# Kernel tuning notes

Measured on AMD Instinct MI355X. Metric: run time of the kernel, lower is better.

## Reference

```python
import jax, jax.numpy as jnp
import numpy as np

N = 65536          # n_pts
K = 16             # n_neighbours
IN_DIM, HID, OUT_DIM = 128, 1024, 32


def setup_inputs() -> dict:
    key = jax.random.key(0)
    ks = jax.random.split(key, 16)

    def lin(k, i, o):
        kw, kb = jax.random.split(k)
        s = 1.0 / np.sqrt(i)
        return (jax.random.uniform(kw, (i, o), jnp.float32, -s, s),
                jax.random.uniform(kb, (o,), jnp.float32, -s, s))

    W1, b1 = lin(ks[0], IN_DIM, HID)
    W2, b2 = lin(ks[1], HID, HID)
    W3, b3 = lin(ks[2], HID, HID // 2)
    W4, b4 = lin(ks[3], HID // 2, OUT_DIM)

    x1 = jax.random.normal(ks[4], (N, IN_DIM), jnp.float32)
    x2 = jax.random.normal(ks[5], (N, IN_DIM), jnp.float32)
    # faiss.knn_gpu outputs (distances, neighbor indices) -- modeled as inputs
    dists1 = jax.random.uniform(ks[6], (N, K), jnp.float32)
    dists2 = jax.random.uniform(ks[7], (N, K), jnp.float32)
    nn_idx1 = jax.random.randint(ks[8], (N, K), 0, N)
    nn_idx2 = jax.random.randint(ks[9], (N, K), 0, N)

    return {"x1": x1, "x2": x2, "dists1": dists1, "nn_idx1": nn_idx1,
            "dists2": dists2, "nn_idx2": nn_idx2,
            "W1": W1, "b1": b1, "W2": W2, "b2": b2,
            "W3": W3, "b3": b3, "W4": W4, "b4": b4}


def _mapper(x, W1, b1, W2, b2, W3, b3, W4, b4):
    h = jax.nn.relu(x @ W1 + b1)
    h = jax.nn.relu(h @ W2 + b2)
    h = jax.nn.relu(h @ W3 + b3)
    return h @ W4 + b4


def _degree(dists, nn_flat, rows_flat):
    # Gaussian edge weights w = exp(-d^2 / (2 sigma^2)), sigma = row mean of d.
    # Symmetrized COO affinity A has entries (nn, row) and (row, nn) each w/2.
    # Row-sum of A (= torch.sparse.sum(A, dim=1)); by symmetry also the col-sum.
    sigma = dists.mean(axis=1, keepdims=True)
    w = jnp.exp(-dists ** 2 / (2.0 * sigma ** 2)).reshape(-1)
    wh = 0.5 * w
    d = (jax.ops.segment_sum(wh, rows_flat, num_segments=N)
         + jax.ops.segment_sum(wh, nn_flat, num_segments=N))
    return d


def reference(x1, x2, dists1, nn_idx1, dists2, nn_idx2,
              W1, b1, W2, b2, W3, b3, W4, b4):
    rows_flat = jnp.repeat(jnp.arange(N, dtype=nn_idx1.dtype), K)
    nn1_flat = nn_idx1.reshape(-1)
    nn2_flat = nn_idx2.reshape(-1)

    # --- ort step on x1 (eval pass) ---
    y1 = _mapper(x1, W1, b1, W2, b2, W3, b3, W4, b4)
    d1 = _degree(dists1, nn1_flat, rows_flat)
    y1 = y1 / d1[:, None]
    gram = y1.T @ y1 + 1e-7 * jnp.eye(OUT_DIM, dtype=y1.dtype)
    L = jnp.linalg.cholesky(gram)
    operator = jnp.linalg.inv(L).T * jnp.asarray(np.sqrt(N), y1.dtype)

    # --- loss pass on x2 ---
    d2 = _degree(dists2, nn2_flat, rows_flat)  # col-sum of affinity A2
    y = _mapper(x2, W1, b1, W2, b2, W3, b3, W4, b4) @ operator
    y = y / d2[:, None]

    # per-edge squared embedding distances ||y_i - y_{nn(i,k)}||^2  [N,K]
    diff = y[:, None, :] - y[nn_idx2]          # [N, K, OUT_DIM]
    de = jnp.sum(diff * diff, axis=-1).reshape(-1)
    # sparse D has entries (nn,row) and (row,nn) each with value de.
    # total sum of A @ D == colsum(A) . rowsum(D)  (duplicates sum in COO).
    rowsum_D = (jax.ops.segment_sum(de, nn2_flat, num_segments=N)
                + jax.ops.segment_sum(de, rows_flat, num_segments=N))
    loss = jnp.dot(d2, rowsum_D) / N
    return loss
```

## Files before the change

kernel.cpp:

```cpp
#include <hip/hip_runtime.h>


#define NPTS  65536
#define KNN   16
#define INDIM 128
#define HID   1024
#define HID2  512
#define ODIM  32
#define ESL   32

typedef unsigned short u16;
typedef unsigned int   u32;
typedef __attribute__((ext_vector_type(8))) short bf16x8;
typedef __attribute__((ext_vector_type(4))) float f32x4;

__device__ __forceinline__ u16 f2bf(float v) {
    union { float f; unsigned u; } x; x.f = v;
    unsigned r = x.u + 0x7fffu + ((x.u >> 16) & 1u);
    return (u16)(r >> 16);
}

__device__ __forceinline__ void gload_lds16(const u16* g, u16* l) {
    __builtin_amdgcn_global_load_lds(
        (const __attribute__((address_space(1))) u32*)g,
        (__attribute__((address_space(3))) u32*)l, 16, 0, 0);
}

template <int N> __device__ __forceinline__ void vmwait() {
    asm volatile("s_waitcnt vmcnt(%0)" :: "n"(N) : "memory");
}
__device__ __forceinline__ void wg_barrier() {
    asm volatile("s_barrier" ::: "memory");
}

__global__ void cvt_bf16_k(const float* __restrict__ in, u16* __restrict__ out, int n4) {
    int i = blockIdx.x * blockDim.x + threadIdx.x;
    if (i >= n4) return;
    float4 v = reinterpret_cast<const float4*>(in)[i];
    unsigned lo = (unsigned)f2bf(v.x) | ((unsigned)f2bf(v.y) << 16);
    unsigned hi = (unsigned)f2bf(v.z) | ((unsigned)f2bf(v.w) << 16);
    reinterpret_cast<uint2*>(out)[i] = make_uint2(lo, hi);
}

__global__ void trans_bf16_k(const float* __restrict__ W, u16* __restrict__ Wt,
                             int rows, int cols) {
    int idx = blockIdx.x * blockDim.x + threadIdx.x;
    if (idx >= rows * cols) return;
    int o = idx / rows, i = idx - o * rows;
    Wt[idx] = f2bf(W[(size_t)i * cols + o]);
}

__global__ void edgew_k(const float* __restrict__ dists1, float* __restrict__ w1,
                        float* __restrict__ dr1,
                        const float* __restrict__ dists2, float* __restrict__ w2,
                        float* __restrict__ dr2) {
    const float* dists = blockIdx.y ? dists2 : dists1;
    float*       wbuf  = blockIdx.y ? w2     : w1;
    float*       drow  = blockIdx.y ? dr2    : dr1;
    int i = blockIdx.x * blockDim.x + threadIdx.x;
    if (i >= NPTS) return;
    const float4* dr = reinterpret_cast<const float4*>(dists + (size_t)i * KNN);
    float4 a = dr[0], b = dr[1], c = dr[2], e = dr[3];
    float buf[KNN] = {a.x,a.y,a.z,a.w,b.x,b.y,b.z,b.w,c.x,c.y,c.z,c.w,e.x,e.y,e.z,e.w};
    float s = 0.f;
    #pragma unroll
    for (int k = 0; k < KNN; ++k) s += buf[k];
    float sigma = s * (1.f / KNN);
    float inv2s2 = 1.f / (2.f * sigma * sigma);
    float w[KNN];
    float rs = 0.f;
    #pragma unroll
    for (int k = 0; k < KNN; ++k) { w[k] = __expf(-buf[k] * buf[k] * inv2s2); rs += w[k]; }
    drow[i] = 0.5f * rs;
    float4* wo = reinterpret_cast<float4*>(wbuf + (size_t)i * KNN);
    wo[0] = make_float4(w[0], w[1], w[2], w[3]);
    wo[1] = make_float4(w[4], w[5], w[6], w[7]);
    wo[2] = make_float4(w[8], w[9], w[10], w[11]);
    wo[3] = make_float4(w[12], w[13], w[14], w[15]);
}

__global__ __launch_bounds__(512) void scatter_k(
    const int* __restrict__ nn1, const float* __restrict__ w1,
    const int* __restrict__ nn2, const float* __restrict__ w2,
    float* __restrict__ partial) {
    __shared__ float bins[16384];
    const int slice = blockIdx.x, range = blockIdx.y, g = blockIdx.z;
    const int* nn   = g ? nn2 : nn1;
    const float* wb = g ? w2  : w1;
    for (int b = threadIdx.x; b < 16384; b += 512) bins[b] = 0.f;
    __syncthreads();
    const int per4  = (NPTS * KNN / ESL) >> 2;
    const int base4 = slice * per4;
    const int4*   nn4 = reinterpret_cast<const int4*>(nn);
    const float4* w4  = reinterpret_cast<const float4*>(wb);
    #pragma unroll 2
    for (int k = 0; k < per4 / 512; ++k) {
        int e4 = base4 + k * 512 + threadIdx.x;
        int4   idx = nn4[e4];
        float4 wv  = w4[e4];
        if ((idx.x >> 14) == range) atomicAdd(&bins[idx.x & 16383], wv.x);
        if ((idx.y >> 14) == range) atomicAdd(&bins[idx.y & 16383], wv.y);
        if ((idx.z >> 14) == range) atomicAdd(&bins[idx.z & 16383], wv.z);
        if ((idx.w >> 14) == range) atomicAdd(&bins[idx.w & 16383], wv.w);
    }
    __syncthreads();
    float* dst = partial + ((size_t)(g * ESL + slice) << 16) + (range << 14);
    for (int b = threadIdx.x; b < 16384; b += 512) dst[b] = bins[b];
}

__global__ __launch_bounds__(256) void dreduce_k(
    const float* __restrict__ partial, float* __restrict__ d1, float* __restrict__ d2) {
    int i = blockIdx.x * 256 + threadIdx.x;
    int g = blockIdx.y;
    const float* p = partial + ((size_t)(g * ESL) << 16) + i;
    float s = 0.f;
    #pragma unroll 8
    for (int sl = 0; sl < ESL; ++sl) s += p[(size_t)sl << 16];
    float* d = g ? d2 : d1;
    d[i] += 0.5f * s;
}

template <int BN, bool RELU>
__global__ __launch_bounds__(512) void gemm256_k(
    const u16* __restrict__ A, const u16* __restrict__ Bt,
    const float* __restrict__ bias, u16* __restrict__ C,
    int M, int Ncols, int Kd)
{
    constexpr int WN   = BN / 4;
    constexpr int NREP = WN / 16;
    constexpr int AL   = 4;
    constexpr int BL   = BN / 64;
    constexpr int LQ   = AL + BL;

    constexpr int A_U16  = 2 * 256 * 64;
    constexpr int B_U16  = 2 * BN * 64;
    constexpr int LDSC   = BN + 16;
    constexpr int EP_U16 = 256 * LDSC;
    constexpr int SM_U16 = (A_U16 + B_U16 > EP_U16) ? (A_U16 + B_U16) : EP_U16;

    __shared__ __attribute__((aligned(16))) u16 smem[SM_U16];
    u16* Asm = smem;
    u16* Bsm = smem + A_U16;

    const int tid  = threadIdx.x;
    const int lane = tid & 63;
    const int wave = tid >> 6;
    const int wr   = wave >> 2;
    const int wc   = wave & 3;
    const int l15  = lane & 15;
    const int kq   = lane >> 4;

    const int nwg = gridDim.x * gridDim.y;
    int sid = blockIdx.y * gridDim.x + blockIdx.x;
    int q = nwg >> 3, r = nwg & 7;
    int xcd = sid & 7, ix = sid >> 3;
    int logical = (xcd < r) ? xcd * (q + 1) + ix
                            : r * (q + 1) + (xcd - r) * q + ix;
    const int m0 = (logical / gridDim.x) * 256;
    const int n0 = (logical % gridDim.x) * BN;

    const int lrow = lane >> 3;
    const int lcol = ((lane & 7) ^ lrow) * 8;

    auto stage = [&](int slot, int kt) {
        #pragma unroll
        for (int j = 0; j < AL; ++j) {
            int seg = wave * AL + j;
            gload_lds16(A + (size_t)(m0 + seg * 8 + lrow) * Kd + kt + lcol,
                        &Asm[slot * 256 * 64 + seg * 512]);
        }
        #pragma unroll
        for (int j = 0; j < BL; ++j) {
            int seg = wave * BL + j;
            gload_lds16(Bt + (size_t)(n0 + seg * 8 + lrow) * Kd + kt + lcol,
                        &Bsm[slot * BN * 64 + seg * 512]);
        }
    };
    auto rdA = [&](int slot, int mi, int ks) -> bf16x8 {
        int row = wr * 128 + mi * 16 + l15;
        int ch  = (ks * 4 + kq) ^ (row & 7);
        return *reinterpret_cast<const bf16x8*>(&Asm[slot * 256 * 64 + row * 64 + ch * 8]);
    };
    auto rdB = [&](int slot, int ni, int ks) -> bf16x8 {
        int row = wc * WN + ni * 16 + l15;
        int ch  = (ks * 4 + kq) ^ (row & 7);
        return *reinterpret_cast<const bf16x8*>(&Bsm[slot * BN * 64 + row * 64 + ch * 8]);
    };

    const int NT = Kd >> 6;
    f32x4 acc[8][NREP] = {};

    stage(0, 0);
    for (int t = 0; t < NT; ++t) {
        const int cur = t & 1;
        if (t + 1 < NT) { stage(cur ^ 1, (t + 1) << 6); vmwait<LQ>(); }
        else            { vmwait<0>(); }
        wg_barrier();

        bf16x8 a[8][2], b[NREP][2];
        #pragma unroll
        for (int mi = 0; mi < 8; ++mi) { a[mi][0] = rdA(cur, mi, 0); a[mi][1] = rdA(cur, mi, 1); }
        #pragma unroll
        for (int ni = 0; ni < NREP; ++ni) { b[ni][0] = rdB(cur, ni, 0); b[ni][1] = rdB(cur, ni, 1); }
        __builtin_amdgcn_s_setprio(1);
        #pragma unroll
        for (int mi = 0; mi < 8; ++mi)
            #pragma unroll
            for (int ni = 0; ni < NREP; ++ni) {
                acc[mi][ni] = __builtin_amdgcn_mfma_f32_16x16x32_bf16(a[mi][0], b[ni][0], acc[mi][ni], 0, 0, 0);
                acc[mi][ni] = __builtin_amdgcn_mfma_f32_16x16x32_bf16(a[mi][1], b[ni][1], acc[mi][ni], 0, 0, 0);
            }
        __builtin_amdgcn_s_setprio(0);
        wg_barrier();
    }

    #pragma unroll
    for (int ni = 0; ni < NREP; ++ni) {
        int col = wc * WN + ni * 16 + l15;
        float bv = bias[n0 + col];
        #pragma unroll
        for (int mi = 0; mi < 8; ++mi)
            #pragma unroll
            for (int r2 = 0; r2 < 4; ++r2) {
                int row = wr * 128 + mi * 16 + kq * 4 + r2;
                float v = acc[mi][ni][r2] + bv;
                if (RELU) v = v > 0.f ? v : 0.f;
                smem[row * LDSC + col] = f2bf(v);
            }
    }
    __syncthreads();
    constexpr int CHUNKS = BN / 8;
    constexpr int ITERS  = 256 * CHUNKS / 512;
    #pragma unroll
    for (int it = 0; it < ITERS; ++it) {
        int task = it * 512 + tid;
        int row  = task / CHUNKS;
        int ch   = task % CHUNKS;
        uint4 v = *reinterpret_cast<const uint4*>(&smem[row * LDSC + ch * 8]);
        *reinterpret_cast<uint4*>(&C[(size_t)(m0 + row) * Ncols + n0 + ch * 8]) = v;
    }
}

__global__ __launch_bounds__(256) void layer4_k(
    const u16* __restrict__ A, const u16* __restrict__ Bt,
    const float* __restrict__ bias, const float* __restrict__ dscale,
    float* __restrict__ Y, int M)
{
    __shared__ __attribute__((aligned(16))) u16 Bs[32 * 520];
    int tid = threadIdx.x;
    #pragma unroll
    for (int j = 0; j < 8; ++j) {
        int cch = tid + j * 256;
        int row = cch >> 6;
        int ko  = (cch & 63) * 8;
        *reinterpret_cast<uint4*>(&Bs[row * 520 + ko]) =
            *reinterpret_cast<const uint4*>(Bt + (size_t)row * 512 + ko);
    }
    __syncthreads();
    int lane = tid & 63, wave = tid >> 6;
    int l15 = lane & 15, kq = lane >> 4;
    int rowb = blockIdx.x * 64 + wave * 16;
    f32x4 acc[2] = {};
    const u16* Arow = A + (size_t)(rowb + l15) * 512;
    #pragma unroll
    for (int ks = 0; ks < 16; ++ks) {
        bf16x8 a = *reinterpret_cast<const bf16x8*>(Arow + ks * 32 + kq * 8);
        #pragma unroll
        for (int ni = 0; ni < 2; ++ni) {
            bf16x8 b = *reinterpret_cast<const bf16x8*>(&Bs[(ni * 16 + l15) * 520 + ks * 32 + kq * 8]);
            acc[ni] = __builtin_amdgcn_mfma_f32_16x16x32_bf16(a, b, acc[ni], 0, 0, 0);
        }
    }
    #pragma unroll
    for (int ni = 0; ni < 2; ++ni) {
        int col = ni * 16 + l15;
        float bv = bias[col];
        #pragma unroll
        for (int r = 0; r < 4; ++r) {
            int rr = rowb + kq * 4 + r;
            float v = acc[ni][r] + bv;
            if (dscale) v /= dscale[rr];
            Y[(size_t)rr * 32 + col] = v;
        }
    }
}

__global__ __launch_bounds__(256) void gram_k(const float* __restrict__ Y,
                                              float* __restrict__ G) {
    __shared__ float ys[8][32];
    const int ROWS = NPTS / 256;
    int base = blockIdx.x * ROWS;
    int tid = threadIdx.x;
    int r = tid >> 3, c0 = (tid & 7) * 4;
    float a0 = 0, a1 = 0, a2 = 0, a3 = 0;
    for (int i0 = 0; i0 < ROWS; i0 += 8) {
        ys[tid >> 5][tid & 31] = Y[(size_t)(base + i0 + (tid >> 5)) * 32 + (tid & 31)];
        __syncthreads();
        #pragma unroll
        for (int q = 0; q < 8; ++q) {
            float yr = ys[q][r];
            a0 += yr * ys[q][c0];     a1 += yr * ys[q][c0 + 1];
            a2 += yr * ys[q][c0 + 2]; a3 += yr * ys[q][c0 + 3];
        }
        __syncthreads();
    }
    atomicAdd(&G[r * 32 + c0], a0);     atomicAdd(&G[r * 32 + c0 + 1], a1);
    atomicAdd(&G[r * 32 + c0 + 2], a2); atomicAdd(&G[r * 32 + c0 + 3], a3);
}

__global__ __launch_bounds__(256) void chol_oper_k(const float* __restrict__ G,
                                                   float* __restrict__ oper) {
    __shared__ double A[32][33];
    __shared__ double xcol[32][33];
    const int t  = threadIdx.x;
    const int j  = t & 31;
    const int i0 = t >> 5;

    #pragma unroll
    for (int q = 0; q < 4; ++q) {
        int i = i0 + q * 8;
        A[i][j] = (double)G[i * 32 + j] + (i == j ? 1e-7 : 0.0);
    }
    __syncthreads();

    for (int k = 0; k < 32; ++k) {
        double akk = A[k][k];
        __syncthreads();
        if (j == k) {
            double s = sqrt(akk);
            #pragma unroll
            for (int q = 0; q < 4; ++q) {
                int i = i0 + q * 8;
                if (i == k)      A[i][k] = s;
                else if (i > k)  A[i][k] /= s;
            }
        }
        __syncthreads();
        if (j > k) {
            double ajk = A[j][k];
            #pragma unroll
            for (int q = 0; q < 4; ++q) {
                int i = i0 + q * 8;
                if (i >= j) A[i][j] -= A[i][k] * ajk;
            }
        }
        __syncthreads();
    }

    const int c = j;
    double s[4] = {0.0, 0.0, 0.0, 0.0};
    for (int jj = 0; jj < 32; ++jj) {
        if (i0 == (jj & 7) && jj >= c) {
            double rhs = (jj == c) ? 1.0 : 0.0;
            xcol[jj][c] = (rhs - s[jj >> 3]) / A[jj][jj];
        }
        __syncthreads();
        if (jj >= c) {
            double x = xcol[jj][c];
            #pragma unroll
            for (int q = 0; q < 4; ++q) {
                int r = i0 + q * 8;
                if (r > jj) s[q] += A[r][jj] * x;
            }
        }
        __syncthreads();
    }
    #pragma unroll
    for (int q = 0; q < 4; ++q) {
        int r = i0 + q * 8;
        oper[c * 32 + r] = (r >= c) ? (float)(xcol[r][c] * 256.0) : 0.f;
    }
}

__global__ __launch_bounds__(256) void apply_oper_k(
    const float* __restrict__ Yr, const float* __restrict__ oper,
    const float* __restrict__ d2, float* __restrict__ Yo) {
    __shared__ float op[1024];
    int tid = threadIdx.x;
    #pragma unroll
    for (int j = tid; j < 1024; j += 256) op[j] = oper[j];
    __syncthreads();
    int idx = blockIdx.x * 256 + tid;
    int i = idx >> 5, j = idx & 31;
    const float* row = Yr + (size_t)i * 32;
    float s = 0.f;
    #pragma unroll
    for (int q = 0; q < 32; ++q) s += row[q] * op[q * 32 + j];
    Yo[idx] = s / d2[i];
}

__global__ __launch_bounds__(256) void loss_k(
    const float* __restrict__ Y, const int* __restrict__ nn,
    const float* __restrict__ d2, double* __restrict__ part) {
    int e = blockIdx.x * 256 + threadIdx.x;
    int i = e >> 4;
    int j = nn[e];
    const float4* yi = reinterpret_cast<const float4*>(Y + (size_t)i * 32);
    const float4* yj = reinterpret_cast<const float4*>(Y + (size_t)j * 32);
    float s = 0.f;
    #pragma unroll
    for (int q = 0; q < 8; ++q) {
        float4 a = yi[q], b = yj[q];
        float dx = a.x - b.x, dy = a.y - b.y, dz = a.z - b.z, dw = a.w - b.w;
        s += dx * dx + dy * dy + dz * dz + dw * dw;
    }
    double local = (double)s * ((double)d2[i] + (double)d2[j]);
    #pragma unroll
    for (int off = 32; off > 0; off >>= 1) local += __shfl_down(local, off);
    __shared__ double wsum[4];
    if ((threadIdx.x & 63) == 0) wsum[threadIdx.x >> 6] = local;
    __syncthreads();
    if (threadIdx.x == 0)
        part[blockIdx.x] = wsum[0] + wsum[1] + wsum[2] + wsum[3];
}

__global__ __launch_bounds__(256) void reduce_part_k(
    const double* __restrict__ part, int n, float* __restrict__ out) {
    double s = 0.0;
    for (int i = threadIdx.x; i < n; i += 256) s += part[i];
    #pragma unroll
    for (int off = 32; off > 0; off >>= 1) s += __shfl_down(s, off);
    __shared__ double wsum[4];
    if ((threadIdx.x & 63) == 0) wsum[threadIdx.x >> 6] = s;
    __syncthreads();
    if (threadIdx.x == 0)
        out[0] = (float)((wsum[0] + wsum[1] + wsum[2] + wsum[3]) / (double)NPTS);
}

extern "C" void kernel_launch(void* const* d_in, const int* in_sizes, int n_in,
                              void* d_out, int out_size, void* d_ws, size_t ws_size,
                              hipStream_t stream) {
    const float* x1     = (const float*)d_in[0];
    const float* x2     = (const float*)d_in[1];
    const float* dists1 = (const float*)d_in[2];
    const int*   nn1    = (const int*)  d_in[3];
    const float* dists2 = (const float*)d_in[4];
    const int*   nn2    = (const int*)  d_in[5];
    const float* W1 = (const float*)d_in[6];  const float* b1 = (const float*)d_in[7];
    const float* W2 = (const float*)d_in[8];  const float* b2 = (const float*)d_in[9];
    const float* W3 = (const float*)d_in[10]; const float* b3 = (const float*)d_in[11];
    const float* W4 = (const float*)d_in[12]; const float* b4 = (const float*)d_in[13];

    char* ws = (char*)d_ws;
    size_t off = 0;
    auto alloc = [&](size_t bytes) { char* p = ws + off; off += (bytes + 255) & ~(size_t)255; return p; };
    u16*    xb   = (u16*)   alloc((size_t)NPTS * INDIM * 2);
    float*  yraw = (float*) alloc((size_t)NPTS * ODIM * 4);
    float*  yop  = (float*) alloc((size_t)NPTS * ODIM * 4);
    u16*    W1t  = (u16*)   alloc((size_t)HID * INDIM * 2);
    u16*    W2t  = (u16*)   alloc((size_t)HID * HID * 2);
    u16*    W3t  = (u16*)   alloc((size_t)HID2 * HID * 2);
    u16*    W4t  = (u16*)   alloc((size_t)ODIM * HID2 * 2);
    float*  d1   = (float*) alloc((size_t)NPTS * 4);
    float*  d2   = (float*) alloc((size_t)NPTS * 4);
    float*  wb1  = (float*) alloc((size_t)NPTS * KNN * 4);
    float*  wb2  = (float*) alloc((size_t)NPTS * KNN * 4);
    float*  dpart= (float*) alloc((size_t)2 * ESL * NPTS * 4);
    float*  gram = (float*) alloc(32 * 32 * 4);
    float*  oper = (float*) alloc(32 * 32 * 4);
    double* part = (double*)alloc((size_t)(NPTS * KNN / 256) * 8);
    size_t fixed = off;
    (void)in_sizes; (void)n_in; (void)out_size;

    int chunk = 2048;
    for (int c = 32768; c >= 2048; c >>= 1)
        if (fixed + (size_t)c * 1024 * 2 * 2 + 512 <= ws_size) { chunk = c; break; }
    u16* cb1 = (u16*)alloc((size_t)chunk * HID * 2);
    u16* cb2 = (u16*)alloc((size_t)chunk * HID * 2);

    trans_bf16_k<<<(INDIM * HID + 255) / 256, 256, 0, stream>>>(W1, W1t, INDIM, HID);
    trans_bf16_k<<<(HID * HID + 255) / 256, 256, 0, stream>>>(W2, W2t, HID, HID);
    trans_bf16_k<<<(HID * HID2 + 255) / 256, 256, 0, stream>>>(W3, W3t, HID, HID2);
    trans_bf16_k<<<(HID2 * ODIM + 255) / 256, 256, 0, stream>>>(W4, W4t, HID2, ODIM);
    hipMemsetAsync(gram, 0, 32 * 32 * 4, stream);

    edgew_k<<<dim3(NPTS / 256, 2), 256, 0, stream>>>(dists1, wb1, d1, dists2, wb2, d2);
    scatter_k<<<dim3(ESL, 4, 2), 512, 0, stream>>>(nn1, wb1, nn2, wb2, dpart);
    dreduce_k<<<dim3(NPTS / 256, 2), 256, 0, stream>>>(dpart, d1, d2);

    dim3 g12(HID / 256, chunk / 256);
    dim3 g3(HID2 / 128, chunk / 256);

    for (int pass = 0; pass < 2; ++pass) {
        const float* x = pass == 0 ? x1 : x2;
        cvt_bf16_k<<<(NPTS * INDIM / 4 + 255) / 256, 256, 0, stream>>>(x, xb, NPTS * INDIM / 4);
        for (int s0 = 0; s0 < NPTS; s0 += chunk) {
            const u16* Ain = xb + (size_t)s0 * INDIM;
            gemm256_k<256, true><<<g12, 512, 0, stream>>>(Ain, W1t, b1, cb1, chunk, HID, INDIM);
            gemm256_k<256, true><<<g12, 512, 0, stream>>>(cb1, W2t, b2, cb2, chunk, HID, HID);
            gemm256_k<128, true><<<g3, 512, 0, stream>>>(cb2, W3t, b3, cb1, chunk, HID2, HID);
            layer4_k<<<chunk / 64, 256, 0, stream>>>(
                cb1, W4t, b4, pass == 0 ? d1 + s0 : nullptr,
                yraw + (size_t)s0 * ODIM, chunk);
        }
        if (pass == 0) {
            gram_k<<<256, 256, 0, stream>>>(yraw, gram);
            chol_oper_k<<<1, 256, 0, stream>>>(gram, oper);
        } else {
            apply_oper_k<<<NPTS * ODIM / 256, 256, 0, stream>>>(yraw, oper, d2, yop);
            loss_k<<<NPTS * KNN / 256, 256, 0, stream>>>(yop, nn2, d2, part);
            reduce_part_k<<<1, 256, 0, stream>>>(part, NPTS * KNN / 256, (float*)d_out);
        }
    }
}
```

Before: 776.9 us.

## Software-pipeline LDS fragment reads with MFMA in quadrant-split GEMM loop

```diff
diff --git a/kernel.cpp b/kernel.cpp
--- a/kernel.cpp
+++ b/kernel.cpp
@@ -120,18 +120,15 @@
     d[i] += 0.5f * s;
 }
 
-template <int BN, bool RELU>
+template <bool RELU>
 __global__ __launch_bounds__(512) void gemm256_k(
     const u16* __restrict__ A, const u16* __restrict__ Bt,
     const float* __restrict__ bias, u16* __restrict__ C,
     int M, int Ncols, int Kd)
 {
-    constexpr int WN   = BN / 4;
-    constexpr int NREP = WN / 16;
+    constexpr int BN   = 256;
     constexpr int AL   = 4;
-    constexpr int BL   = BN / 64;
-    constexpr int LQ   = AL + BL;
-
+    constexpr int BL   = 4;
     constexpr int A_U16  = 2 * 256 * 64;
     constexpr int B_U16  = 2 * BN * 64;
     constexpr int LDSC   = BN + 16;
@@ -182,41 +179,79 @@
         return *reinterpret_cast<const bf16x8*>(&Asm[slot * 256 * 64 + row * 64 + ch * 8]);
     };
     auto rdB = [&](int slot, int ni, int ks) -> bf16x8 {
-        int row = wc * WN + ni * 16 + l15;
+        int row = wc * 64 + ni * 16 + l15;
         int ch  = (ks * 4 + kq) ^ (row & 7);
         return *reinterpret_cast<const bf16x8*>(&Bsm[slot * BN * 64 + row * 64 + ch * 8]);
     };
 
     const int NT = Kd >> 6;
-    f32x4 acc[8][NREP] = {};
+    f32x4 acc[8][4] = {};
+    bf16x8 alo[4][2], ahi[4][2], blo[2][2], bhi[2][2];
 
     stage(0, 0);
+    vmwait<0>();
+    wg_barrier();
+    #pragma unroll
+    for (int mi = 0; mi < 4; ++mi) { alo[mi][0] = rdA(0, mi, 0); alo[mi][1] = rdA(0, mi, 1); }
+    #pragma unroll
+    for (int ni = 0; ni < 2; ++ni) { blo[ni][0] = rdB(0, ni, 0); blo[ni][1] = rdB(0, ni, 1); }
+
     for (int t = 0; t < NT; ++t) {
         const int cur = t & 1;
-        if (t + 1 < NT) { stage(cur ^ 1, (t + 1) << 6); vmwait<LQ>(); }
-        else            { vmwait<0>(); }
-        wg_barrier();
-
-        bf16x8 a[8][2], b[NREP][2];
-        #pragma unroll
-        for (int mi = 0; mi < 8; ++mi) { a[mi][0] = rdA(cur, mi, 0); a[mi][1] = rdA(cur, mi, 1); }
-        #pragma unroll
-        for (int ni = 0; ni < NREP; ++ni) { b[ni][0] = rdB(cur, ni, 0); b[ni][1] = rdB(cur, ni, 1); }
+        if (t + 1 < NT) stage(cur ^ 1, (t + 1) << 6);
+        #pragma unroll
+        for (int ni = 0; ni < 2; ++ni) { bhi[ni][0] = rdB(cur, ni + 2, 0); bhi[ni][1] = rdB(cur, ni + 2, 1); }
         __builtin_amdgcn_s_setprio(1);
         #pragma unroll
-        for (int mi = 0; mi < 8; ++mi)
-            #pragma unroll
-            for (int ni = 0; ni < NREP; ++ni) {
-                acc[mi][ni] = __builtin_amdgcn_mfma_f32_16x16x32_bf16(a[mi][0], b[ni][0], acc[mi][ni], 0, 0, 0);
-                acc[mi][ni] = __builtin_amdgcn_mfma_f32_16x16x32_bf16(a[mi][1], b[ni][1], acc[mi][ni], 0, 0, 0);
+        for (int mi = 0; mi < 4; ++mi)
+            #pragma unroll
+            for (int ni = 0; ni < 2; ++ni) {
+                acc[mi][ni] = __builtin_amdgcn_mfma_f32_16x16x32_bf16(alo[mi][0], blo[ni][0], acc[mi][ni], 0, 0, 0);
+                acc[mi][ni] = __builtin_amdgcn_mfma_f32_16x16x32_bf16(alo[mi][1], blo[ni][1], acc[mi][ni], 0, 0, 0);
             }
         __builtin_amdgcn_s_setprio(0);
-        wg_barrier();
-    }
-
-    #pragma unroll
-    for (int ni = 0; ni < NREP; ++ni) {
-        int col = wc * WN + ni * 16 + l15;
+        #pragma unroll
+        for (int mi = 0; mi < 4; ++mi) { ahi[mi][0] = rdA(cur, mi + 4, 0); ahi[mi][1] = rdA(cur, mi + 4, 1); }
+        __builtin_amdgcn_s_setprio(1);
+        #pragma unroll
+        for (int mi = 0; mi < 4; ++mi)
+            #pragma unroll
+            for (int ni = 0; ni < 2; ++ni) {
+                acc[mi][ni + 2] = __builtin_amdgcn_mfma_f32_16x16x32_bf16(alo[mi][0], bhi[ni][0], acc[mi][ni + 2], 0, 0, 0);
+                acc[mi][ni + 2] = __builtin_amdgcn_mfma_f32_16x16x32_bf16(alo[mi][1], bhi[ni][1], acc[mi][ni + 2], 0, 0, 0);
+            }
+        __builtin_amdgcn_s_setprio(0);
+        __builtin_amdgcn_s_setprio(1);
+        #pragma unroll
+        for (int mi = 0; mi < 4; ++mi)
+            #pragma unroll
+            for (int ni = 0; ni < 2; ++ni) {
+                acc[mi + 4][ni] = __builtin_amdgcn_mfma_f32_16x16x32_bf16(ahi[mi][0], blo[ni][0], acc[mi + 4][ni], 0, 0, 0);
+                acc[mi + 4][ni] = __builtin_amdgcn_mfma_f32_16x16x32_bf16(ahi[mi][1], blo[ni][1], acc[mi + 4][ni], 0, 0, 0);
+            }
+        __builtin_amdgcn_s_setprio(0);
+        if (t + 1 < NT) { vmwait<0>(); wg_barrier(); }
+        __builtin_amdgcn_s_setprio(1);
+        #pragma unroll
+        for (int mi = 0; mi < 4; ++mi)
+            #pragma unroll
+            for (int ni = 0; ni < 2; ++ni) {
+                acc[mi + 4][ni + 2] = __builtin_amdgcn_mfma_f32_16x16x32_bf16(ahi[mi][0], bhi[ni][0], acc[mi + 4][ni + 2], 0, 0, 0);
+                acc[mi + 4][ni + 2] = __builtin_amdgcn_mfma_f32_16x16x32_bf16(ahi[mi][1], bhi[ni][1], acc[mi + 4][ni + 2], 0, 0, 0);
+            }
+        __builtin_amdgcn_s_setprio(0);
+        if (t + 1 < NT) {
+            #pragma unroll
+            for (int mi = 0; mi < 4; ++mi) { alo[mi][0] = rdA(cur ^ 1, mi, 0); alo[mi][1] = rdA(cur ^ 1, mi, 1); }
+            #pragma unroll
+            for (int ni = 0; ni < 2; ++ni) { blo[ni][0] = rdB(cur ^ 1, ni, 0); blo[ni][1] = rdB(cur ^ 1, ni, 1); }
+        }
+    }
+
+    __syncthreads();
+    #pragma unroll
+    for (int ni = 0; ni < 4; ++ni) {
+        int col = wc * 64 + ni * 16 + l15;
         float bv = bias[n0 + col];
         #pragma unroll
         for (int mi = 0; mi < 8; ++mi)
@@ -479,16 +514,16 @@
     dreduce_k<<<dim3(NPTS / 256, 2), 256, 0, stream>>>(dpart, d1, d2);
 
     dim3 g12(HID / 256, chunk / 256);
-    dim3 g3(HID2 / 128, chunk / 256);
+    dim3 g3(HID2 / 256, chunk / 256);
 
     for (int pass = 0; pass < 2; ++pass) {
         const float* x = pass == 0 ? x1 : x2;
         cvt_bf16_k<<<(NPTS * INDIM / 4 + 255) / 256, 256, 0, stream>>>(x, xb, NPTS * INDIM / 4);
         for (int s0 = 0; s0 < NPTS; s0 += chunk) {
             const u16* Ain = xb + (size_t)s0 * INDIM;
-            gemm256_k<256, true><<<g12, 512, 0, stream>>>(Ain, W1t, b1, cb1, chunk, HID, INDIM);
-            gemm256_k<256, true><<<g12, 512, 0, stream>>>(cb1, W2t, b2, cb2, chunk, HID, HID);
-            gemm256_k<128, true><<<g3, 512, 0, stream>>>(cb2, W3t, b3, cb1, chunk, HID2, HID);
+            gemm256_k<true><<<g12, 512, 0, stream>>>(Ain, W1t, b1, cb1, chunk, HID, INDIM);
+            gemm256_k<true><<<g12, 512, 0, stream>>>(cb1, W2t, b2, cb2, chunk, HID, HID);
+            gemm256_k<true><<<g3, 512, 0, stream>>>(cb2, W3t, b3, cb1, chunk, HID2, HID);
             layer4_k<<<chunk / 64, 256, 0, stream>>>(
                 cb1, W4t, b4, pass == 0 ? d1 + s0 : nullptr,
                 yraw + (size_t)s0 * ODIM, chunk);
```

Measured after the change: 731.2 us. 5.9% less time.
